# Kernel tuning notes

Measured on AMD Instinct MI355X. Metric: run time of the kernel, lower is better.

The kernel has to match this reference:

```python
import jax, jax.numpy as jnp
import numpy as np

NUM_NODES = 1048576
NUM_FEAT = 128
HIDDEN = 64
NUM_GRAPHS = 4096
OUT_DIM = 5


def setup_inputs() -> dict:
    key = jax.random.key(0)
    ks = jax.random.split(key, 8)
    x = jax.random.normal(ks[0], (NUM_NODES, NUM_FEAT), dtype=jnp.float32)
    batch = jnp.sort(jax.random.randint(ks[1], (NUM_NODES,), 0, NUM_GRAPHS, dtype=jnp.int64))
    s1 = 1.0 / np.sqrt(NUM_FEAT)
    s2 = 1.0 / np.sqrt(HIDDEN)
    W1 = jax.random.uniform(ks[2], (NUM_FEAT, HIDDEN), jnp.float32, -s1, s1)
    b1 = jax.random.uniform(ks[3], (HIDDEN,), jnp.float32, -s1, s1)
    W2 = jax.random.uniform(ks[4], (HIDDEN, HIDDEN), jnp.float32, -s2, s2)
    b2 = jax.random.uniform(ks[5], (HIDDEN,), jnp.float32, -s2, s2)
    W3 = jax.random.uniform(ks[6], (HIDDEN, OUT_DIM), jnp.float32, -s2, s2)
    b3 = jax.random.uniform(ks[7], (OUT_DIM,), jnp.float32, -s2, s2)
    return {"x": x, "batch": batch, "W1": W1, "b1": b1, "W2": W2, "b2": b2, "W3": W3, "b3": b3}


def reference(x, batch, W1, b1, W2, b2, W3, b3):
    # Segment-mean pooling over nodes -> [NUM_GRAPHS, NUM_FEAT]
    sums = jax.ops.segment_sum(x, batch, num_segments=NUM_GRAPHS)
    counts = jax.ops.segment_sum(jnp.ones((x.shape[0],), x.dtype), batch, num_segments=NUM_GRAPHS)
    pooled = jnp.where(counts[:, None] > 0, sums / jnp.maximum(counts, 1.0)[:, None], jnp.zeros((), x.dtype))
    # MLP head: feat -> hidden -> hidden -> 5
    h = jax.nn.relu(pooled @ W1 + b1)
    h = jax.nn.relu(h @ W2 + b2)
    return h @ W3 + b3
```

## Files before the change

kernel.cpp:

```cpp
#include <hip/hip_runtime.h>

#define NUM_NODES  1048576
#define NUM_FEAT   128
#define HIDDEN     64
#define NUM_GRAPHS 4096
#define OUT_DIM    5

typedef float f32x4 __attribute__((ext_vector_type(4)));

__global__ __launch_bounds__(256) void seg_scan_kernel(
    const int* __restrict__ batch, int* __restrict__ seg)
{
    const int i = blockIdx.x * blockDim.x + threadIdx.x;
    if (i >= NUM_NODES) return;
    const int b = batch[i];
    const int prev = (i == 0) ? -1 : batch[i - 1];
    for (int g = prev + 1; g <= b; ++g) seg[g] = i;
    if (i == NUM_NODES - 1) {
        for (int g = b + 1; g <= NUM_GRAPHS; ++g) seg[g] = NUM_NODES;
    }
}

__global__ __launch_bounds__(128, 8) void gcn_fused_kernel(
    const float* __restrict__ x,
    const int*   __restrict__ seg,
    const float* __restrict__ W1, const float* __restrict__ b1,
    const float* __restrict__ W2, const float* __restrict__ b2,
    const float* __restrict__ W3, const float* __restrict__ b3,
    float* __restrict__ out)
{
    const int g = blockIdx.x;
    const int t = threadIdx.x;

    const int start = seg[g];
    const int end   = seg[g + 1];
    const int count = end - start;

    const int cg = t & 31;
    const int ro = t >> 5;

    int iters = count - ro + 3;
    iters = (iters > 0) ? (iters >> 2) : 0;

    const f32x4* p = reinterpret_cast<const f32x4*>(
        x + (size_t)(start + ro) * NUM_FEAT) + cg;
    const int step = NUM_FEAT;

    f32x4 acc0 = (f32x4)0.0f, acc1 = (f32x4)0.0f;
    int i = 0;
    for (; i + 2 <= iters; i += 2) {
        const f32x4 v0 = __builtin_nontemporal_load(p);
        const f32x4 v1 = __builtin_nontemporal_load(p + step);
        acc0 += v0;
        acc1 += v1;
        p += 2 * step;
    }
    if (i < iters) {
        acc0 += __builtin_nontemporal_load(p);
    }
    f32x4 acc = acc0 + acc1;

    __shared__ f32x4 part[128];
    __shared__ float pooled[NUM_FEAT];
    __shared__ float h1[HIDDEN];
    __shared__ float h2[HIDDEN];

    part[t] = acc;
    __syncthreads();

    if (t < 32) {
        f32x4 s = part[t] + part[t + 32] + part[t + 64] + part[t + 96];
        const float inv = (count > 0) ? (1.0f / (float)count) : 0.0f;
        pooled[t * 4 + 0] = s.x * inv;
        pooled[t * 4 + 1] = s.y * inv;
        pooled[t * 4 + 2] = s.z * inv;
        pooled[t * 4 + 3] = s.w * inv;
    }
    __syncthreads();

    if (t < HIDDEN) {
        float s = b1[t];
        #pragma unroll 8
        for (int k = 0; k < NUM_FEAT; ++k) s = fmaf(pooled[k], W1[k * HIDDEN + t], s);
        h1[t] = fmaxf(s, 0.0f);
    }
    __syncthreads();

    if (t < HIDDEN) {
        float s = b2[t];
        #pragma unroll 8
        for (int k = 0; k < HIDDEN; ++k) s = fmaf(h1[k], W2[k * HIDDEN + t], s);
        h2[t] = fmaxf(s, 0.0f);
    }
    __syncthreads();

    if (t < OUT_DIM) {
        float s = b3[t];
        #pragma unroll 8
        for (int k = 0; k < HIDDEN; ++k) s = fmaf(h2[k], W3[k * OUT_DIM + t], s);
        out[g * OUT_DIM + t] = s;
    }
}

extern "C" void kernel_launch(void* const* d_in, const int* in_sizes, int n_in,
                              void* d_out, int out_size, void* d_ws, size_t ws_size,
                              hipStream_t stream) {
    const float* x     = (const float*)d_in[0];
    const int*   batch = (const int*)d_in[1];
    const float* W1    = (const float*)d_in[2];
    const float* b1    = (const float*)d_in[3];
    const float* W2    = (const float*)d_in[4];
    const float* b2    = (const float*)d_in[5];
    const float* W3    = (const float*)d_in[6];
    const float* b3    = (const float*)d_in[7];
    float* out = (float*)d_out;

    int* seg = (int*)d_ws;

    seg_scan_kernel<<<NUM_NODES / 256, 256, 0, stream>>>(batch, seg);
    gcn_fused_kernel<<<NUM_GRAPHS, 128, 0, stream>>>(x, seg, W1, b1, W2, b2, W3, b3, out);
}
```

Baseline: 99.09 us.

## Find segment bounds by wave-wide search and split the MLP into a batched kernel

Removes the separate segment-scan kernel. Each pool block now finds its own start and end by a 64-way ballot search over the sorted batch array. The MLP head moves into a second kernel that stages the weights in shared memory once per block and handles 16 graphs per block. This is meant to cut the per-graph global weight reads and the serial tail on 64 threads, at the cost of a round trip for the pooled buffer through global memory and extra launch and search latency.

```diff
diff --git a/kernel.cpp b/kernel.cpp
--- a/kernel.cpp
+++ b/kernel.cpp
@@ -8,37 +8,45 @@
 
 typedef float f32x4 __attribute__((ext_vector_type(4)));
 
-__global__ __launch_bounds__(256) void seg_scan_kernel(
-    const int* __restrict__ batch, int* __restrict__ seg)
-{
-    const int i = blockIdx.x * blockDim.x + threadIdx.x;
-    if (i >= NUM_NODES) return;
-    const int b = batch[i];
-    const int prev = (i == 0) ? -1 : batch[i - 1];
-    for (int g = prev + 1; g <= b; ++g) seg[g] = i;
-    if (i == NUM_NODES - 1) {
-        for (int g = b + 1; g <= NUM_GRAPHS; ++g) seg[g] = NUM_NODES;
-    }
-}
-
-__global__ __launch_bounds__(128, 8) void gcn_fused_kernel(
+__global__ __launch_bounds__(128, 8) void pool_kernel(
     const float* __restrict__ x,
-    const int*   __restrict__ seg,
-    const float* __restrict__ W1, const float* __restrict__ b1,
-    const float* __restrict__ W2, const float* __restrict__ b2,
-    const float* __restrict__ W3, const float* __restrict__ b3,
-    float* __restrict__ out)
+    const int*   __restrict__ batch,
+    float* __restrict__ pooled)
 {
     const int g = blockIdx.x;
     const int t = threadIdx.x;
+    const int lane = t & 63;
+    const int T = g + (t >> 6);
 
-    const int start = seg[g];
-    const int end   = seg[g + 1];
+    int lo = 0, hi = NUM_NODES;
+    while (hi - lo > 64) {
+        const int w = hi - lo;
+        const int base = lo;
+        const int pos = base + (int)(((long long)w * lane) >> 6);
+        const unsigned long long bal = __ballot(batch[pos] < T);
+        const int m = __popcll(bal);
+        if (m == 0) {
+            hi = lo;
+        } else {
+            lo = base + (int)(((long long)w * (m - 1)) >> 6) + 1;
+            if (m < 64) hi = base + (int)(((long long)w * m) >> 6);
+        }
+    }
+    if (hi > lo) {
+        const int w = hi - lo;
+        const bool pred = (lane < w) ? (batch[lo + lane] < T) : false;
+        lo += __popcll(__ballot(pred));
+    }
+
+    __shared__ int bounds[2];
+    if (lane == 0) bounds[t >> 6] = lo;
+    __syncthreads();
+    const int start = bounds[0];
+    const int end   = bounds[1];
     const int count = end - start;
 
     const int cg = t & 31;
     const int ro = t >> 5;
-
     int iters = count - ro + 3;
     iters = (iters > 0) ? (iters >> 2) : 0;
 
@@ -55,50 +63,78 @@
         acc1 += v1;
         p += 2 * step;
     }
-    if (i < iters) {
-        acc0 += __builtin_nontemporal_load(p);
-    }
-    f32x4 acc = acc0 + acc1;
+    if (i < iters) acc0 += __builtin_nontemporal_load(p);
 
     __shared__ f32x4 part[128];
-    __shared__ float pooled[NUM_FEAT];
-    __shared__ float h1[HIDDEN];
-    __shared__ float h2[HIDDEN];
-
-    part[t] = acc;
+    part[t] = acc0 + acc1;
     __syncthreads();
 
     if (t < 32) {
         f32x4 s = part[t] + part[t + 32] + part[t + 64] + part[t + 96];
         const float inv = (count > 0) ? (1.0f / (float)count) : 0.0f;
-        pooled[t * 4 + 0] = s.x * inv;
-        pooled[t * 4 + 1] = s.y * inv;
-        pooled[t * 4 + 2] = s.z * inv;
-        pooled[t * 4 + 3] = s.w * inv;
+        s *= inv;
+        *(reinterpret_cast<f32x4*>(pooled + (size_t)g * NUM_FEAT) + t) = s;
     }
+}
+
+__global__ __launch_bounds__(256) void mlp_kernel(
+    const float* __restrict__ pooled,
+    const float* __restrict__ W1, const float* __restrict__ b1,
+    const float* __restrict__ W2, const float* __restrict__ b2,
+    const float* __restrict__ W3, const float* __restrict__ b3,
+    float* __restrict__ out)
+{
+    __shared__ float W1s[NUM_FEAT * HIDDEN];
+    __shared__ float W2s[HIDDEN * HIDDEN];
+    __shared__ float W3s[HIDDEN * OUT_DIM];
+    __shared__ float b1s[HIDDEN], b2s[HIDDEN], b3s[OUT_DIM];
+    __shared__ float pr[4][NUM_FEAT];
+    __shared__ float h1s[4][HIDDEN], h2s[4][HIDDEN];
+
+    const int t = threadIdx.x;
+
+    for (int i = t; i < NUM_FEAT * HIDDEN / 4; i += 256)
+        ((f32x4*)W1s)[i] = ((const f32x4*)W1)[i];
+    for (int i = t; i < HIDDEN * HIDDEN / 4; i += 256)
+        ((f32x4*)W2s)[i] = ((const f32x4*)W2)[i];
+    for (int i = t; i < HIDDEN * OUT_DIM; i += 256)
+        W3s[i] = W3[i];
+    if (t < HIDDEN) { b1s[t] = b1[t]; b2s[t] = b2[t]; }
+    if (t < OUT_DIM) b3s[t] = b3[t];
     __syncthreads();
 
-    if (t < HIDDEN) {
-        float s = b1[t];
+    const int gbase = blockIdx.x * 16;
+    for (int it = 0; it < 4; ++it) {
+        const int g0 = gbase + it * 4;
+
+        if (t < 128) {
+            const int row = t >> 5, e = t & 31;
+            ((f32x4*)pr[row])[e] =
+                *(reinterpret_cast<const f32x4*>(pooled + (size_t)(g0 + row) * NUM_FEAT) + e);
+        }
+        __syncthreads();
+
+        const int q = t >> 6, h = t & 63;
+        float s = b1s[h];
         #pragma unroll 8
-        for (int k = 0; k < NUM_FEAT; ++k) s = fmaf(pooled[k], W1[k * HIDDEN + t], s);
-        h1[t] = fmaxf(s, 0.0f);
-    }
-    __syncthreads();
+        for (int k = 0; k < NUM_FEAT; ++k) s = fmaf(pr[q][k], W1s[k * HIDDEN + h], s);
+        h1s[q][h] = fmaxf(s, 0.0f);
+        __syncthreads();
 
-    if (t < HIDDEN) {
-        float s = b2[t];
+        s = b2s[h];
         #pragma unroll 8
-        for (int k = 0; k < HIDDEN; ++k) s = fmaf(h1[k], W2[k * HIDDEN + t], s);
-        h2[t] = fmaxf(s, 0.0f);
-    }
-    __syncthreads();
+        for (int k = 0; k < HIDDEN; ++k) s = fmaf(h1s[q][k], W2s[k * HIDDEN + h], s);
+        h2s[q][h] = fmaxf(s, 0.0f);
+        __syncthreads();
 
-    if (t < OUT_DIM) {
-        float s = b3[t];
-        #pragma unroll 8
-        for (int k = 0; k < HIDDEN; ++k) s = fmaf(h2[k], W3[k * OUT_DIM + t], s);
-        out[g * OUT_DIM + t] = s;
+        if (t < 4 * OUT_DIM) {
+            const int qq = t / OUT_DIM, o = t % OUT_DIM;
+            float so = b3s[o];
+            #pragma unroll 8
+            for (int k = 0; k < HIDDEN; ++k) so = fmaf(h2s[qq][k], W3s[k * OUT_DIM + o], so);
+            out[(size_t)(g0 + qq) * OUT_DIM + o] = so;
+        }
+        __syncthreads();
     }
 }
 
@@ -115,8 +151,8 @@
     const float* b3    = (const float*)d_in[7];
     float* out = (float*)d_out;
 
-    int* seg = (int*)d_ws;
+    float* pooled = (float*)d_ws;
 
-    seg_scan_kernel<<<NUM_NODES / 256, 256, 0, stream>>>(batch, seg);
-    gcn_fused_kernel<<<NUM_GRAPHS, 128, 0, stream>>>(x, seg, W1, b1, W2, b2, W3, b3, out);
+    pool_kernel<<<NUM_GRAPHS, 128, 0, stream>>>(x, batch, pooled);
+    mlp_kernel<<<NUM_GRAPHS / 16, 256, 0, stream>>>(pooled, W1, b1, W2, b2, W3, b3, out);
 }
```

Measured after the change: 109.8 us. 1.11x slower.
